# Performance work log

Hardware: AMD Instinct MI355X
Metric: run time of the kernel (lower is better)

Reference implementation:

```python
import jax, jax.numpy as jnp
import numpy as np

TWO_PI = 2.0 * np.pi
ALPHA = 0.65
KSIZE = (3, 3, 3)   # (kOr, kH, kW)
ITERS = 1
BN_EPS = 1e-5


def _interp(v, dy, dx):
    """Bilinear sample of v[b,c,o, y+dy[o], x+dx[o]], border-clamped.
    v: [B,C,Or,H,W]; dy, dx: [Or] float per-orientation constant shifts."""
    H, W = v.shape[3], v.shape[4]
    y0 = jnp.floor(dy); fy = dy - y0; y0 = y0.astype(jnp.int32)
    iy = jnp.arange(H)[None, :] + y0[:, None]                      # [Or,H]
    g0 = jnp.take_along_axis(v, jnp.clip(iy, 0, H - 1)[None, None, :, :, None], axis=3)
    g1 = jnp.take_along_axis(v, jnp.clip(iy + 1, 0, H - 1)[None, None, :, :, None], axis=3)
    fyb = fy[None, None, :, None, None]
    v = (1.0 - fyb) * g0 + fyb * g1
    x0 = jnp.floor(dx); fx = dx - x0; x0 = x0.astype(jnp.int32)
    ix = jnp.arange(W)[None, :] + x0[:, None]                      # [Or,W]
    h0 = jnp.take_along_axis(v, jnp.clip(ix, 0, W - 1)[None, None, :, None, :], axis=4)
    h1 = jnp.take_along_axis(v, jnp.clip(ix + 1, 0, W - 1)[None, None, :, None, :], axis=4)
    fxb = fx[None, None, :, None, None]
    return (1.0 - fxb) * h0 + fxb * h1


def _convection(u, g0):
    """out[b,c,p] = u[b,c, p . g0[c]^{-1}] via trilinear resampling.
    Sample point: ((x,y) - R(theta - th0)@(x0,y0), theta - th0), theta periodic."""
    Or = u.shape[2]
    def one(uc, g):  # uc: [B,Or,H,W], g = (x0, y0, th0)
        x0, y0, th0 = g[0], g[1], g[2]
        t = th0 * Or / TWO_PI
        i = jnp.floor(t); f = t - i; i = i.astype(jnp.int32)
        # periodic linear interpolation along orientation axis
        v = (1.0 - f) * jnp.roll(uc, i, axis=1) + f * jnp.roll(uc, i + 1, axis=1)
        a = jnp.arange(Or, dtype=u.dtype) * (TWO_PI / Or) - th0
        dx = -(jnp.cos(a) * x0 - jnp.sin(a) * y0)
        dy = -(jnp.sin(a) * x0 + jnp.cos(a) * y0)
        return _interp(v[:, None], dy, dx)[:, 0]
    return jax.vmap(one, in_axes=(1, 0), out_axes=1)(u, g0)


def _se2_log(qx, qy, dth):
    """Exact SE(2) logarithm coordinates (c1,c2,c3) of group offset (qx,qy,dth)."""
    if abs(dth) < 1e-9:
        return qx, qy, dth
    h = 0.5 * dth
    cot = np.cos(h) / np.sin(h)
    return h * (qx * cot + qy), h * (-qx + qy * cot), dth


def _morph(u, metric, dilate):
    """Fractional morphological dilation (max of u(p.q) - k(q)) or erosion
    (min of u(p.q) + k(q)) with left-invariant Riemannian kernel
    k_c(q) = nu_a * d_c(q)^{2a/(2a-1)}, d_c^2 = (m0*c1)^2+(m1*c2)^2+(m2*c3)^2."""
    kOr, kH, kW = KSIZE
    Or = u.shape[2]
    thetas = jnp.arange(Or, dtype=u.dtype) * (TWO_PI / Or)
    p = 2.0 * ALPHA / (2.0 * ALPHA - 1.0)
    nu = (2.0 * ALPHA - 1.0) * (2.0 * ALPHA) ** (-p)
    out = None
    for qt in range(-(kOr // 2), kOr // 2 + 1):
        dth = qt * TWO_PI / Or
        for qy in range(-(kH // 2), kH // 2 + 1):
            for qx in range(-(kW // 2), kW // 2 + 1):
                c1, c2, c3 = _se2_log(float(qx), float(qy), dth)
                s = (metric[:, 0] * c1) ** 2 + (metric[:, 1] * c2) ** 2 + (metric[:, 2] * c3) ** 2
                k = nu * s ** (p / 2.0)                       # [C]
                # left-invariant shift: spatial offset rotated by theta_o
                dxo = jnp.cos(thetas) * qx - jnp.sin(thetas) * qy
                dyo = jnp.sin(thetas) * qx + jnp.cos(thetas) * qy
                val = _interp(jnp.roll(u, -qt, axis=2), dyo, dxo)
                kb = k[None, :, None, None, None]
                cand = val - kb if dilate else val + kb
                if out is None:
                    out = cand
                else:
                    out = jnp.maximum(out, cand) if dilate else jnp.minimum(out, cand)
    return out


def setup_inputs() -> dict:
    key = jax.random.key(0)
    ks = jax.random.split(key, 5)
    B, Cin, Cout, Or, H, W = 4, 8, 16, 8, 128, 128
    x = jax.random.normal(ks[0], (B, Cin, Or, H, W), dtype=jnp.float32)
    g0 = 0.5 * jax.random.normal(ks[1], (Cin, 3), dtype=jnp.float32)
    lo, hi = 1.4 / 3.0, 0.7 * 3.0   # reset_parameters range for metric params
    metric_dil = jax.random.uniform(ks[2], (Cin, 3), minval=lo, maxval=hi, dtype=jnp.float32)
    metric_ero = jax.random.uniform(ks[3], (Cin, 3), minval=lo, maxval=hi, dtype=jnp.float32)
    bound = 0.25  # kaiming_uniform(a=sqrt(5)) bound for [8,16] weight
    weight = jax.random.uniform(ks[4], (Cin, Cout), minval=-bound, maxval=bound, dtype=jnp.float32)
    gamma = jnp.ones((Cout,), jnp.float32)
    beta = jnp.zeros((Cout,), jnp.float32)
    return dict(x=x, g0=g0, metric_dil=metric_dil, metric_ero=metric_ero,
                weight=weight, gamma=gamma, beta=beta)


def reference(x, g0, metric_dil, metric_ero, weight, gamma, beta):
    u = x
    for _ in range(ITERS):
        u = _convection(u, g0)
        u = _morph(u, metric_dil, dilate=True)
        u = _morph(u, metric_ero, dilate=False)
    # channel mixing: [B,Cin,Or,H,W] x [Cin,Cout] -> [B,Cout,Or,H,W]
    y = jnp.einsum('bcohw,cd->bdohw', u, weight)
    # BatchNorm3d (training mode): per-channel stats over (B,Or,H,W)
    m = y.mean(axis=(0, 2, 3, 4), keepdims=True)
    v = y.var(axis=(0, 2, 3, 4), keepdims=True)
    yh = (y - m) * jax.lax.rsqrt(v + BN_EPS)
    return yh * gamma[None, :, None, None, None] + beta[None, :, None, None, None]
```

## Files before the change

kernel.cpp:

```cpp
#include <hip/hip_runtime.h>
#include <math.h>
#include <utility>

#define B 4
#define CIN 8
#define COUT 16
#define OR_ 8
#define H_ 128
#define W_ 128
#define HW 16384
#define PLANE HW
#define CH_STR (OR_*HW)
#define BATCH_STR (CIN*CH_STR)
#define NELEM (B*BATCH_STR)
#define NPOS (B*OR_*HW)
#define NB_RED 512

#define PROW 132
#define PPLANE (132*132)
#define NPLANES (B*CIN*OR_)
#define PAD_CELLS 1040

typedef __attribute__((ext_vector_type(4))) float f4;
typedef __attribute__((ext_vector_type(2))) float f2;

struct Tables {
  float kdil[CIN][27];
  float kero[CIN][27];
  int   conv_i[CIN];
  float conv_f[CIN];
  float conv_dy[CIN][OR_];
  float conv_dx[CIN][OR_];
};

__host__ __device__ constexpr double m_cos(int o) {
  const double r = 0.70710678118654752440;
  const double t[8] = {1.0, r, 0.0, -r, -1.0, -r, 0.0, r};
  return t[o];
}
__host__ __device__ constexpr double m_sin(int o) {
  const double r = 0.70710678118654752440;
  const double t[8] = {0.0, r, 1.0, r, 0.0, -r, -1.0, -r};
  return t[o];
}
__host__ __device__ constexpr double tap_dx(int o, int j) {
  return m_cos(o)*(j % 3 - 1) - m_sin(o)*(j / 3 - 1);
}
__host__ __device__ constexpr double tap_dy(int o, int j) {
  return m_sin(o)*(j % 3 - 1) + m_cos(o)*(j / 3 - 1);
}
__host__ __device__ constexpr int ifloor(double v) {
  int i = (int)v;
  return ((double)i > v) ? i - 1 : i;
}
__host__ __device__ constexpr int tap_ix(int o, int j) { return ifloor(tap_dx(o, j)); }
__host__ __device__ constexpr int tap_iy(int o, int j) { return ifloor(tap_dy(o, j)); }
__host__ __device__ constexpr float tap_fx(int o, int j) { return (float)(tap_dx(o, j) - tap_ix(o, j)); }
__host__ __device__ constexpr float tap_fy(int o, int j) { return (float)(tap_dy(o, j) - tap_iy(o, j)); }
__host__ __device__ constexpr float corner_w(int o, int j, int dyb, int dxb) {
  float fy = tap_fy(o, j), fx = tap_fx(o, j);
  return (dyb ? fy : 1.0f - fy) * (dxb ? fx : 1.0f - fx);
}
__host__ __device__ constexpr int corner_r(int o, int j, int dyb) { return tap_iy(o, j) + dyb + 2; }
__host__ __device__ constexpr int corner_c(int o, int j, int i, int dxb) { return i + tap_ix(o, j) + dxb + 2; }
__host__ __device__ constexpr bool row_used(int o, int r) {
  for (int j = 0; j < 9; ++j)
    for (int dyb = 0; dyb < 2; ++dyb)
      for (int dxb = 0; dxb < 2; ++dxb)
        if (corner_w(o, j, dyb, dxb) != 0.0f && corner_r(o, j, dyb) == r)
          return true;
  return false;
}

template<int N> struct Rep {
  template<class F> __device__ __forceinline__ static void run(F&& f) {
    Rep<N-1>::run(f);
    f(std::integral_constant<int, N-1>{});
  }
};
template<> struct Rep<0> {
  template<class F> __device__ __forceinline__ static void run(F&&) {}
};


__global__ void precompute_kernel(const float* __restrict__ g0,
                                  const float* __restrict__ mdil,
                                  const float* __restrict__ mero,
                                  Tables* __restrict__ T) {
  const int t = threadIdx.x;
  const double TWO_PI = 6.283185307179586476925286766559;
  const double P  = 2.0*0.65/(2.0*0.65 - 1.0);
  const double NU = (2.0*0.65 - 1.0)*pow(2.0*0.65, -P);
  if (t < 432) {
    int which = t / 216;
    int r = t % 216;
    int c = r / 27;
    int j = r % 27;
    int qt = j/9 - 1;
    int qy = (j/3)%3 - 1;
    int qx = j%3 - 1;
    double dth = qt * (TWO_PI/OR_);
    double c1, c2, c3;
    if (qt == 0) { c1 = qx; c2 = qy; c3 = 0.0; }
    else {
      double h = 0.5*dth;
      double cot = cos(h)/sin(h);
      c1 = h*(qx*cot + qy);
      c2 = h*(-qx + qy*cot);
      c3 = dth;
    }
    const float* m = which ? mero : mdil;
    double a0 = (double)m[c*3+0]*c1;
    double a1 = (double)m[c*3+1]*c2;
    double a2 = (double)m[c*3+2]*c3;
    double s = a0*a0 + a1*a1 + a2*a2;
    float k = (float)(NU * pow(s, P*0.5));
    if (which) T->kero[c][j] = k; else T->kdil[c][j] = k;
  } else if (t >= 512 && t < 512 + CIN*OR_) {
    int r = t - 512;
    int c = r / OR_;
    int o = r % OR_;
    float x0 = g0[c*3+0], y0 = g0[c*3+1], th0 = g0[c*3+2];
    float a = (float)(o*(TWO_PI/OR_)) - th0;
    float ca = cosf(a), sa = sinf(a);
    T->conv_dx[c][o] = -(ca*x0 - sa*y0);
    T->conv_dy[c][o] = -(sa*x0 + ca*y0);
    if (o == 0) {
      float tt = th0 * (float)(OR_/TWO_PI);
      float fi = floorf(tt);
      T->conv_i[c] = (int)fi;
      T->conv_f[c] = tt - fi;
    }
  }
}

__global__ void conv_kernel(const float* __restrict__ x, float* __restrict__ out,
                            const Tables* __restrict__ T) {
  int idx = blockIdx.x*256 + threadIdx.x;
  int w = idx & 127;
  int h = (idx >> 7) & 127;
  int o = (idx >> 14) & 7;
  int c = (idx >> 17) & 7;
  int b = idx >> 20;
  int i = T->conv_i[c];
  float f = T->conv_f[c];
  int o1 = (o - i) & 7;
  int o2 = (o - i - 1) & 7;
  const float* p1 = x + b*BATCH_STR + c*CH_STR + o1*PLANE;
  const float* p2 = x + b*BATCH_STR + c*CH_STR + o2*PLANE;
  float dy = T->conv_dy[c][o], dx = T->conv_dx[c][o];
  float fy0 = floorf(dy); float fy = dy - fy0;
  float fx0 = floorf(dx); float fx = dx - fx0;
  int iy = h + (int)fy0;
  int ix = w + (int)fx0;
  int r0 = min(max(iy, 0), 127), r1 = min(max(iy+1, 0), 127);
  int c0 = min(max(ix, 0), 127), c1 = min(max(ix+1, 0), 127);
  float w00 = (1.f-fy)*(1.f-fx), w01 = (1.f-fy)*fx, w10 = fy*(1.f-fx), w11 = fy*fx;
  float v1 = w00*p1[r0*W_+c0] + w01*p1[r0*W_+c1] + w10*p1[r1*W_+c0] + w11*p1[r1*W_+c1];
  float v2 = w00*p2[r0*W_+c0] + w01*p2[r0*W_+c1] + w10*p2[r1*W_+c0] + w11*p2[r1*W_+c1];
  int pl = ((b*CIN + c)*OR_ + o);
  out[pl*PPLANE + (h+2)*PROW + (w+2)] = (1.0f - f)*v1 + f*v2;
}

__global__ void pad_kernel(float* __restrict__ t) {
  int i = blockIdx.x*256 + threadIdx.x;
  if (i >= NPLANES*PAD_CELLS) return;
  int plane = i / PAD_CELLS;
  int r = i - plane*PAD_CELLS;
  int pr, pc;
  if (r < 4*PROW) {
    int rr = r / PROW;
    pc = r - rr*PROW;
    pr = (rr < 2) ? rr : rr + 128;
  } else {
    int j = r - 4*PROW;
    pr = 2 + (j >> 2);
    int cc = j & 3;
    pc = (cc < 2) ? cc : cc + 128;
  }
  int lh = min(max(pr - 2, 0), 127);
  int lw = min(max(pc - 2, 0), 127);
  float v = t[plane*PPLANE + (lh+2)*PROW + (lw+2)];
  t[plane*PPLANE + pr*PROW + pc] = v;
}

template<int O, int DIL>
__device__ __forceinline__ void morph_plane(const float* __restrict__ prow0,
                                            const float* __restrict__ kq,
                                            float acc[4]) {
  float win[5][8];
  Rep<5>::run([&](auto rc) {
    constexpr int r = decltype(rc)::value;
    if constexpr (row_used(O, r)) {
      const f4* p = (const f4*)(prow0 + r*PROW);
      f4 lo = p[0], hi = p[1];
      win[r][0] = lo.x; win[r][1] = lo.y; win[r][2] = lo.z; win[r][3] = lo.w;
      win[r][4] = hi.x; win[r][5] = hi.y; win[r][6] = hi.z; win[r][7] = hi.w;
    }
  });
  Rep<9>::run([&](auto jc) {
    constexpr int j = decltype(jc)::value;
    float k = kq[j];
    float base = DIL ? -k : k;
    Rep<4>::run([&](auto ic) {
      constexpr int i = decltype(ic)::value;
      float v = base;
      Rep<4>::run([&](auto cc2) {
        constexpr int cn  = decltype(cc2)::value;
        constexpr int dyb = cn >> 1, dxb = cn & 1;
        constexpr float Wgt = corner_w(O, j, dyb, dxb);
        if constexpr (Wgt != 0.0f) {
          constexpr int R = corner_r(O, j, dyb);
          constexpr int C = corner_c(O, j, i, dxb);
          v = fmaf(Wgt, win[R][C], v);
        }
      });
      acc[i] = DIL ? fmaxf(acc[i], v) : fminf(acc[i], v);
    });
  });
}

template<int O, int DIL>
__device__ __forceinline__ void morph_body4(const float* __restrict__ base,
                                            const float* __restrict__ kt,
                                            int h, int w0, float acc[4]) {
  Rep<3>::run([&](auto qc) {
    constexpr int qti = decltype(qc)::value;
    const float* plane = base + ((O + qti + 7) & 7) * PPLANE;
    morph_plane<O, DIL>(plane + h*PROW + w0, kt + qti*9, acc);
  });
}

template<int DIL>
__global__ void morph_kernel(const float* __restrict__ in, float* __restrict__ out,
                             const Tables* __restrict__ T) {
  int i4 = blockIdx.x*256 + threadIdx.x;
  int w0 = (i4 & 31) << 2;
  int h  = (i4 >> 5) & 127;
  int o  = (i4 >> 12) & 7;
  int c  = (i4 >> 15) & 7;
  int b  = i4 >> 18;
  const float* base = in + (b*CIN + c)*(OR_*PPLANE);
  const float* kt = DIL ? T->kdil[c] : T->kero[c];
  float acc[4];
  #pragma unroll
  for (int i = 0; i < 4; ++i) acc[i] = DIL ? -INFINITY : INFINITY;
  switch (o) {
    case 0: morph_body4<0, DIL>(base, kt, h, w0, acc); break;
    case 1: morph_body4<1, DIL>(base, kt, h, w0, acc); break;
    case 2: morph_body4<2, DIL>(base, kt, h, w0, acc); break;
    case 3: morph_body4<3, DIL>(base, kt, h, w0, acc); break;
    case 4: morph_body4<4, DIL>(base, kt, h, w0, acc); break;
    case 5: morph_body4<5, DIL>(base, kt, h, w0, acc); break;
    case 6: morph_body4<6, DIL>(base, kt, h, w0, acc); break;
    default: morph_body4<7, DIL>(base, kt, h, w0, acc); break;
  }
  if (DIL) {
    float* dst = out + ((b*CIN + c)*OR_ + o)*PPLANE + (h+2)*PROW + (w0+2);
    f2 a = {acc[0], acc[1]}, bb = {acc[2], acc[3]};
    *(f2*)dst = a;
    *(f2*)(dst + 2) = bb;
  } else {
    float* dst = out + (((b*CIN + c)*OR_ + o)*PLANE) + h*W_ + w0;
    f4 v = {acc[0], acc[1], acc[2], acc[3]};
    *(f4*)dst = v;
  }
}

__global__ void gram_kernel(const float* __restrict__ u, double* __restrict__ part) {
  int t4 = blockIdx.x*256 + threadIdx.x;
  int hw = (t4 & 4095) << 2;
  int o  = (t4 >> 12) & 7;
  int b  = t4 >> 15;
  const float* base = u + b*BATCH_STR + o*PLANE + hw;
  f4 v[8];
  #pragma unroll
  for (int c = 0; c < 8; c++) v[c] = *(const f4*)(base + c*CH_STR);
  float S[8], G[36];
  #pragma unroll
  for (int c = 0; c < 8; c++) S[c] = v[c].x + v[c].y + v[c].z + v[c].w;
  {
    int t = 0;
    #pragma unroll
    for (int c = 0; c < 8; c++)
      #pragma unroll
      for (int c2 = c; c2 < 8; c2++) {
        G[t] = v[c].x*v[c2].x + v[c].y*v[c2].y + v[c].z*v[c2].z + v[c].w*v[c2].w;
        t++;
      }
  }
  __shared__ double lds[4][44];
  int lane = threadIdx.x & 63;
  int wave = threadIdx.x >> 6;
  for (int t = 0; t < 44; t++) {
    double vv = (double)((t < 8) ? S[t] : G[t-8]);
    for (int off = 32; off; off >>= 1) vv += __shfl_down(vv, off);
    if (lane == 0) lds[wave][t] = vv;
  }
  __syncthreads();
  if (threadIdx.x < 44) {
    part[blockIdx.x*44 + threadIdx.x] =
      lds[0][threadIdx.x] + lds[1][threadIdx.x] + lds[2][threadIdx.x] + lds[3][threadIdx.x];
  }
}

__global__ void stats_kernel(const double* __restrict__ part, const float* __restrict__ weight,
                             const float* __restrict__ gamma, const float* __restrict__ beta,
                             float* __restrict__ ss) {
  __shared__ double tot[44];
  int t = threadIdx.x;
  if (t < 44) {
    double s = 0.0;
    for (int bidx = 0; bidx < NB_RED; bidx++) s += part[bidx*44 + t];
    tot[t] = s;
  }
  __syncthreads();
  if (t < 16) {
    double m = 0.0;
    for (int c = 0; c < 8; c++) m += (double)weight[c*COUT + t] * tot[c];
    double e2 = 0.0;
    int idx = 8;
    for (int c = 0; c < 8; c++)
      for (int c2 = c; c2 < 8; c2++) {
        double wp = (double)weight[c*COUT + t] * (double)weight[c2*COUT + t];
        e2 += (c2 == c ? 1.0 : 2.0) * wp * tot[idx];
        idx++;
      }
    double N = (double)NPOS;
    m /= N; e2 /= N;
    double var = e2 - m*m;
    double inv = rsqrt(var + 1e-5);
    float sc = (float)(inv * (double)gamma[t]);
    ss[t]      = sc;
    ss[16 + t] = beta[t] - (float)m * sc;
  }
}

__global__ void final_kernel(const float* __restrict__ u, const float* __restrict__ weight,
                             const float* __restrict__ ss, float* __restrict__ out) {
  __shared__ float Wsh[8][16];
  __shared__ float scale[16], shift[16];
  int t = threadIdx.x;
  if (t < 128) Wsh[t >> 4][t & 15] = weight[t];
  if (t < 16) { scale[t] = ss[t]; shift[t] = ss[16 + t]; }
  __syncthreads();
  int t4 = blockIdx.x*256 + threadIdx.x;
  int hw = (t4 & 4095) << 2;
  int o  = (t4 >> 12) & 7;
  int b  = t4 >> 15;
  const float* base = u + b*BATCH_STR + o*PLANE + hw;
  f4 v[8];
  #pragma unroll
  for (int c = 0; c < 8; c++) v[c] = *(const f4*)(base + c*CH_STR);
  float* ob = out + b*(COUT*CH_STR) + o*PLANE + hw;
  #pragma unroll
  for (int d = 0; d < 16; d++) {
    f4 y = {0.f, 0.f, 0.f, 0.f};
    #pragma unroll
    for (int c = 0; c < 8; c++) {
      float wv = Wsh[c][d];
      y.x = fmaf(v[c].x, wv, y.x);
      y.y = fmaf(v[c].y, wv, y.y);
      y.z = fmaf(v[c].z, wv, y.z);
      y.w = fmaf(v[c].w, wv, y.w);
    }
    float sc = scale[d], sh = shift[d];
    f4 r = { fmaf(y.x, sc, sh), fmaf(y.y, sc, sh), fmaf(y.z, sc, sh), fmaf(y.w, sc, sh) };
    *(f4*)(ob + d*CH_STR) = r;
  }
}

extern "C" void kernel_launch(void* const* d_in, const int* in_sizes, int n_in,
                              void* d_out, int out_size, void* d_ws, size_t ws_size,
                              hipStream_t stream) {
  const float* x      = (const float*)d_in[0];
  const float* g0     = (const float*)d_in[1];
  const float* mdil   = (const float*)d_in[2];
  const float* mero   = (const float*)d_in[3];
  const float* weight = (const float*)d_in[4];
  const float* gamma  = (const float*)d_in[5];
  const float* beta   = (const float*)d_in[6];
  float* out = (float*)d_out;

  char* ws = (char*)d_ws;
  Tables* T    = (Tables*)ws;
  float*  ss   = (float*)(ws + 8*1024);
  double* part = (double*)(ws + 16*1024);
  float*  u1p  = (float*)(ws + (size_t)1*1024*1024);
  float*  u2p  = (float*)(ws + (size_t)40*1024*1024);
  float*  u3   = (float*)(ws + (size_t)80*1024*1024);

  const int padBlocks = (NPLANES*PAD_CELLS + 255)/256;

  precompute_kernel<<<1, 1024, 0, stream>>>(g0, mdil, mero, T);
  conv_kernel<<<NELEM/256, 256, 0, stream>>>(x, u1p, T);
  pad_kernel<<<padBlocks, 256, 0, stream>>>(u1p);
  morph_kernel<1><<<NELEM/4/256, 256, 0, stream>>>(u1p, u2p, T);
  pad_kernel<<<padBlocks, 256, 0, stream>>>(u2p);
  morph_kernel<0><<<NELEM/4/256, 256, 0, stream>>>(u2p, u3, T);
  gram_kernel<<<NB_RED, 256, 0, stream>>>(u3, part);
  stats_kernel<<<1, 64, 0, stream>>>(part, weight, gamma, beta, ss);
  final_kernel<<<NPOS/4/256, 256, 0, stream>>>(u3, weight, ss, out);
}
```

Baseline: 128.1 us.

## Fuse convection, dilation and erosion into one LDS-tiled kernel

Replaces the separate convection, two padding and two morphology kernels with a single kernel per 16x16 spatial tile, batch and channel. The convected tile plus a 4-pixel halo is kept in shared memory, dilated into a second shared buffer, border-clamped in place for edge tiles, then eroded and written to global memory. This removes the padded intermediate tensors and their global-memory round trips and launches. In exchange the halo regions are recomputed redundantly, and the larger shared-memory footprint may limit occupancy.

```diff
diff --git a/kernel.cpp b/kernel.cpp
--- a/kernel.cpp
+++ b/kernel.cpp
@@ -16,13 +16,15 @@
 #define NPOS (B*OR_*HW)
 #define NB_RED 512
 
-#define PROW 132
-#define PPLANE (132*132)
-#define NPLANES (B*CIN*OR_)
-#define PAD_CELLS 1040
+#define TILE 16
+#define CB_DIM 24
+#define CB_S   28
+#define CB_PL  (CB_DIM*CB_S)
+#define DB_DIM 20
+#define DB_S   28
+#define DB_PL  (DB_DIM*DB_S)
 
 typedef __attribute__((ext_vector_type(4))) float f4;
-typedef __attribute__((ext_vector_type(2))) float f2;
 
 struct Tables {
   float kdil[CIN][27];
@@ -134,136 +136,163 @@
   }
 }
 
-__global__ void conv_kernel(const float* __restrict__ x, float* __restrict__ out,
-                            const Tables* __restrict__ T) {
-  int idx = blockIdx.x*256 + threadIdx.x;
-  int w = idx & 127;
-  int h = (idx >> 7) & 127;
-  int o = (idx >> 14) & 7;
-  int c = (idx >> 17) & 7;
-  int b = idx >> 20;
-  int i = T->conv_i[c];
-  float f = T->conv_f[c];
-  int o1 = (o - i) & 7;
-  int o2 = (o - i - 1) & 7;
-  const float* p1 = x + b*BATCH_STR + c*CH_STR + o1*PLANE;
-  const float* p2 = x + b*BATCH_STR + c*CH_STR + o2*PLANE;
-  float dy = T->conv_dy[c][o], dx = T->conv_dx[c][o];
-  float fy0 = floorf(dy); float fy = dy - fy0;
-  float fx0 = floorf(dx); float fx = dx - fx0;
-  int iy = h + (int)fy0;
-  int ix = w + (int)fx0;
-  int r0 = min(max(iy, 0), 127), r1 = min(max(iy+1, 0), 127);
-  int c0 = min(max(ix, 0), 127), c1 = min(max(ix+1, 0), 127);
-  float w00 = (1.f-fy)*(1.f-fx), w01 = (1.f-fy)*fx, w10 = fy*(1.f-fx), w11 = fy*fx;
-  float v1 = w00*p1[r0*W_+c0] + w01*p1[r0*W_+c1] + w10*p1[r1*W_+c0] + w11*p1[r1*W_+c1];
-  float v2 = w00*p2[r0*W_+c0] + w01*p2[r0*W_+c1] + w10*p2[r1*W_+c0] + w11*p2[r1*W_+c1];
-  int pl = ((b*CIN + c)*OR_ + o);
-  out[pl*PPLANE + (h+2)*PROW + (w+2)] = (1.0f - f)*v1 + f*v2;
-}
-
-__global__ void pad_kernel(float* __restrict__ t) {
-  int i = blockIdx.x*256 + threadIdx.x;
-  if (i >= NPLANES*PAD_CELLS) return;
-  int plane = i / PAD_CELLS;
-  int r = i - plane*PAD_CELLS;
-  int pr, pc;
-  if (r < 4*PROW) {
-    int rr = r / PROW;
-    pc = r - rr*PROW;
-    pr = (rr < 2) ? rr : rr + 128;
-  } else {
-    int j = r - 4*PROW;
-    pr = 2 + (j >> 2);
-    int cc = j & 3;
-    pc = (cc < 2) ? cc : cc + 128;
-  }
-  int lh = min(max(pr - 2, 0), 127);
-  int lw = min(max(pc - 2, 0), 127);
-  float v = t[plane*PPLANE + (lh+2)*PROW + (lw+2)];
-  t[plane*PPLANE + pr*PROW + pc] = v;
-}
-
-template<int O, int DIL>
-__device__ __forceinline__ void morph_plane(const float* __restrict__ prow0,
-                                            const float* __restrict__ kq,
-                                            float acc[4]) {
-  float win[5][8];
-  Rep<5>::run([&](auto rc) {
-    constexpr int r = decltype(rc)::value;
-    if constexpr (row_used(O, r)) {
-      const f4* p = (const f4*)(prow0 + r*PROW);
-      f4 lo = p[0], hi = p[1];
-      win[r][0] = lo.x; win[r][1] = lo.y; win[r][2] = lo.z; win[r][3] = lo.w;
-      win[r][4] = hi.x; win[r][5] = hi.y; win[r][6] = hi.z; win[r][7] = hi.w;
-    }
-  });
-  Rep<9>::run([&](auto jc) {
-    constexpr int j = decltype(jc)::value;
-    float k = kq[j];
-    float base = DIL ? -k : k;
-    Rep<4>::run([&](auto ic) {
-      constexpr int i = decltype(ic)::value;
-      float v = base;
-      Rep<4>::run([&](auto cc2) {
-        constexpr int cn  = decltype(cc2)::value;
-        constexpr int dyb = cn >> 1, dxb = cn & 1;
-        constexpr float Wgt = corner_w(O, j, dyb, dxb);
-        if constexpr (Wgt != 0.0f) {
-          constexpr int R = corner_r(O, j, dyb);
-          constexpr int C = corner_c(O, j, i, dxb);
-          v = fmaf(Wgt, win[R][C], v);
-        }
+template<int O, int DIL, int PLSTR, int RSTR>
+__device__ __forceinline__ void morph_tile_lds(const float* __restrict__ src,
+                                               const float* __restrict__ kt,
+                                               int row, int gc, float acc[4]) {
+  Rep<3>::run([&](auto qc) {
+    constexpr int qti = decltype(qc)::value;
+    const float* p = src + ((O + qti + 7) & 7) * PLSTR + row * RSTR + gc;
+    float win[5][8];
+    Rep<5>::run([&](auto rc) {
+      constexpr int r = decltype(rc)::value;
+      if constexpr (row_used(O, r)) {
+        f4 lo = *(const f4*)(p + r*RSTR);
+        f4 hi = *(const f4*)(p + r*RSTR + 4);
+        win[r][0] = lo.x; win[r][1] = lo.y; win[r][2] = lo.z; win[r][3] = lo.w;
+        win[r][4] = hi.x; win[r][5] = hi.y; win[r][6] = hi.z; win[r][7] = hi.w;
+      }
+    });
+    Rep<9>::run([&](auto jc) {
+      constexpr int j = decltype(jc)::value;
+      float k = kt[qti*9 + j];
+      float base = DIL ? -k : k;
+      Rep<4>::run([&](auto ic) {
+        constexpr int i = decltype(ic)::value;
+        float v = base;
+        Rep<4>::run([&](auto cc2) {
+          constexpr int cn  = decltype(cc2)::value;
+          constexpr int dyb = cn >> 1, dxb = cn & 1;
+          constexpr float Wgt = corner_w(O, j, dyb, dxb);
+          if constexpr (Wgt != 0.0f) {
+            constexpr int R = corner_r(O, j, dyb);
+            constexpr int C = corner_c(O, j, i, dxb);
+            v = fmaf(Wgt, win[R][C], v);
+          }
+        });
+        acc[i] = DIL ? fmaxf(acc[i], v) : fminf(acc[i], v);
       });
-      acc[i] = DIL ? fmaxf(acc[i], v) : fminf(acc[i], v);
     });
   });
 }
 
-template<int O, int DIL>
-__device__ __forceinline__ void morph_body4(const float* __restrict__ base,
-                                            const float* __restrict__ kt,
-                                            int h, int w0, float acc[4]) {
-  Rep<3>::run([&](auto qc) {
-    constexpr int qti = decltype(qc)::value;
-    const float* plane = base + ((O + qti + 7) & 7) * PPLANE;
-    morph_plane<O, DIL>(plane + h*PROW + w0, kt + qti*9, acc);
-  });
-}
-
-template<int DIL>
-__global__ void morph_kernel(const float* __restrict__ in, float* __restrict__ out,
-                             const Tables* __restrict__ T) {
-  int i4 = blockIdx.x*256 + threadIdx.x;
-  int w0 = (i4 & 31) << 2;
-  int h  = (i4 >> 5) & 127;
-  int o  = (i4 >> 12) & 7;
-  int c  = (i4 >> 15) & 7;
-  int b  = i4 >> 18;
-  const float* base = in + (b*CIN + c)*(OR_*PPLANE);
-  const float* kt = DIL ? T->kdil[c] : T->kero[c];
-  float acc[4];
-  #pragma unroll
-  for (int i = 0; i < 4; ++i) acc[i] = DIL ? -INFINITY : INFINITY;
-  switch (o) {
-    case 0: morph_body4<0, DIL>(base, kt, h, w0, acc); break;
-    case 1: morph_body4<1, DIL>(base, kt, h, w0, acc); break;
-    case 2: morph_body4<2, DIL>(base, kt, h, w0, acc); break;
-    case 3: morph_body4<3, DIL>(base, kt, h, w0, acc); break;
-    case 4: morph_body4<4, DIL>(base, kt, h, w0, acc); break;
-    case 5: morph_body4<5, DIL>(base, kt, h, w0, acc); break;
-    case 6: morph_body4<6, DIL>(base, kt, h, w0, acc); break;
-    default: morph_body4<7, DIL>(base, kt, h, w0, acc); break;
-  }
-  if (DIL) {
-    float* dst = out + ((b*CIN + c)*OR_ + o)*PPLANE + (h+2)*PROW + (w0+2);
-    f2 a = {acc[0], acc[1]}, bb = {acc[2], acc[3]};
-    *(f2*)dst = a;
-    *(f2*)(dst + 2) = bb;
-  } else {
-    float* dst = out + (((b*CIN + c)*OR_ + o)*PLANE) + h*W_ + w0;
-    f4 v = {acc[0], acc[1], acc[2], acc[3]};
-    *(f4*)dst = v;
+template<int O>
+__device__ __forceinline__ void dil_wave(const float* __restrict__ cb, float* __restrict__ db,
+                                         const float* __restrict__ kt, int lane) {
+  #pragma unroll
+  for (int it = 0; it < 2; ++it) {
+    int g = lane + it*64;
+    if (g < 100) {
+      int row = g / 5;
+      int gc = (g - row*5) * 4;
+      float acc[4] = {-INFINITY, -INFINITY, -INFINITY, -INFINITY};
+      morph_tile_lds<O, 1, CB_PL, CB_S>(cb, kt, row, gc, acc);
+      f4 v = {acc[0], acc[1], acc[2], acc[3]};
+      *(f4*)(db + O*DB_PL + row*DB_S + gc) = v;
+    }
+  }
+}
+
+template<int O>
+__device__ __forceinline__ void ero_wave(const float* __restrict__ db, float* __restrict__ dst,
+                                         const float* __restrict__ kt, int lane) {
+  int row = lane >> 2;
+  int gc = (lane & 3) * 4;
+  float acc[4] = {INFINITY, INFINITY, INFINITY, INFINITY};
+  morph_tile_lds<O, 0, DB_PL, DB_S>(db, kt, row, gc, acc);
+  f4 v = {acc[0], acc[1], acc[2], acc[3]};
+  *(f4*)(dst + O*PLANE + row*W_ + gc) = v;
+}
+
+__global__ __launch_bounds__(512, 4)
+void fused_kernel(const float* __restrict__ x, float* __restrict__ u3,
+                  const Tables* __restrict__ T) {
+  __shared__ float convbuf[8*CB_PL];
+  __shared__ float dilbuf[8*DB_PL];
+  int blk = blockIdx.x;
+  int tx = blk & 7, ty = (blk >> 3) & 7, c = (blk >> 6) & 7, b = blk >> 9;
+  int h0 = ty*TILE, w0 = tx*TILE;
+  int t = threadIdx.x;
+  int wid = t >> 6, lane = t & 63;
+
+  const int   ci = T->conv_i[c];
+  const float cf = T->conv_f[c];
+  const float* xc = x + b*BATCH_STR + c*CH_STR;
+  #pragma unroll
+  for (int k = 0; k < 9; ++k) {
+    int cc = t + k*512;
+    int col = cc % CB_DIM;
+    int tmp = cc / CB_DIM;
+    int r = tmp % CB_DIM;
+    int o = tmp / CB_DIM;
+    int gh = min(max(h0 - 4 + r, 0), 127);
+    int gw = min(max(w0 - 4 + col, 0), 127);
+    int o1 = (o - ci) & 7, o2 = (o - ci - 1) & 7;
+    const float* p1 = xc + o1*PLANE;
+    const float* p2 = xc + o2*PLANE;
+    float dy = T->conv_dy[c][o], dx = T->conv_dx[c][o];
+    float fy0 = floorf(dy); float fy = dy - fy0;
+    float fx0 = floorf(dx); float fx = dx - fx0;
+    int iy = gh + (int)fy0;
+    int ix = gw + (int)fx0;
+    int r0 = min(max(iy, 0), 127), r1 = min(max(iy+1, 0), 127);
+    int c0 = min(max(ix, 0), 127), c1 = min(max(ix+1, 0), 127);
+    float w00 = (1.f-fy)*(1.f-fx), w01 = (1.f-fy)*fx, w10 = fy*(1.f-fx), w11 = fy*fx;
+    float v1 = w00*p1[r0*W_+c0] + w01*p1[r0*W_+c1] + w10*p1[r1*W_+c0] + w11*p1[r1*W_+c1];
+    float v2 = w00*p2[r0*W_+c0] + w01*p2[r0*W_+c1] + w10*p2[r1*W_+c0] + w11*p2[r1*W_+c1];
+    convbuf[(o*CB_DIM + r)*CB_S + col] = (1.0f - cf)*v1 + cf*v2;
+  }
+  __syncthreads();
+
+  {
+    const float* kt = T->kdil[c];
+    switch (wid) {
+      case 0: dil_wave<0>(convbuf, dilbuf, kt, lane); break;
+      case 1: dil_wave<1>(convbuf, dilbuf, kt, lane); break;
+      case 2: dil_wave<2>(convbuf, dilbuf, kt, lane); break;
+      case 3: dil_wave<3>(convbuf, dilbuf, kt, lane); break;
+      case 4: dil_wave<4>(convbuf, dilbuf, kt, lane); break;
+      case 5: dil_wave<5>(convbuf, dilbuf, kt, lane); break;
+      case 6: dil_wave<6>(convbuf, dilbuf, kt, lane); break;
+      default: dil_wave<7>(convbuf, dilbuf, kt, lane); break;
+    }
+  }
+  __syncthreads();
+
+  if ((h0 == 0) | (h0 == 112) | (w0 == 0) | (w0 == 112)) {
+    #pragma unroll
+    for (int k = 0; k < 7; ++k) {
+      int cc = t + k*512;
+      if (cc < 3200) {
+        int col = cc % DB_DIM;
+        int tmp = cc / DB_DIM;
+        int row = tmp % DB_DIM;
+        int o = tmp / DB_DIM;
+        int vh = h0 - 2 + row, vw = w0 - 2 + col;
+        int dr = min(max(vh, 0), 127) - vh;
+        int dc = min(max(vw, 0), 127) - vw;
+        if ((dr != 0) | (dc != 0)) {
+          dilbuf[(o*DB_DIM + row)*DB_S + col] =
+            dilbuf[(o*DB_DIM + row + dr)*DB_S + col + dc];
+        }
+      }
+    }
+  }
+  __syncthreads();
+
+  {
+    const float* kt = T->kero[c];
+    float* dst = u3 + (b*CIN + c)*(OR_*PLANE) + h0*W_ + w0;
+    switch (wid) {
+      case 0: ero_wave<0>(dilbuf, dst, kt, lane); break;
+      case 1: ero_wave<1>(dilbuf, dst, kt, lane); break;
+      case 2: ero_wave<2>(dilbuf, dst, kt, lane); break;
+      case 3: ero_wave<3>(dilbuf, dst, kt, lane); break;
+      case 4: ero_wave<4>(dilbuf, dst, kt, lane); break;
+      case 5: ero_wave<5>(dilbuf, dst, kt, lane); break;
+      case 6: ero_wave<6>(dilbuf, dst, kt, lane); break;
+      default: ero_wave<7>(dilbuf, dst, kt, lane); break;
+    }
   }
 }
 
@@ -386,18 +415,10 @@
   Tables* T    = (Tables*)ws;
   float*  ss   = (float*)(ws + 8*1024);
   double* part = (double*)(ws + 16*1024);
-  float*  u1p  = (float*)(ws + (size_t)1*1024*1024);
-  float*  u2p  = (float*)(ws + (size_t)40*1024*1024);
-  float*  u3   = (float*)(ws + (size_t)80*1024*1024);
-
-  const int padBlocks = (NPLANES*PAD_CELLS + 255)/256;
+  float*  u3   = (float*)(ws + (size_t)1*1024*1024);
 
   precompute_kernel<<<1, 1024, 0, stream>>>(g0, mdil, mero, T);
-  conv_kernel<<<NELEM/256, 256, 0, stream>>>(x, u1p, T);
-  pad_kernel<<<padBlocks, 256, 0, stream>>>(u1p);
-  morph_kernel<1><<<NELEM/4/256, 256, 0, stream>>>(u1p, u2p, T);
-  pad_kernel<<<padBlocks, 256, 0, stream>>>(u2p);
-  morph_kernel<0><<<NELEM/4/256, 256, 0, stream>>>(u2p, u3, T);
+  fused_kernel<<<B*CIN*64, 512, 0, stream>>>(x, u3, T);
   gram_kernel<<<NB_RED, 256, 0, stream>>>(u3, part);
   stats_kernel<<<1, 64, 0, stream>>>(part, weight, gamma, beta, ss);
   final_kernel<<<NPOS/4/256, 256, 0, stream>>>(u3, weight, ss, out);
```

Result: faster. 119.5 us (-6.7%).
